# Kernel tuning notes

Measured on AMD Instinct MI355X. Metric: run time of the kernel, lower is better.

The kernel has to match this reference:

```python
import jax, jax.numpy as jnp
import numpy as np

CONF_THRES = 0.8
NMS_THRES = 0.4
MAX_DET = 300          # fixed capacity for jit-compatible NMS output
N_BOXES = 262144
N_CLASSES = 80


def xywh2xyxy(x):
    xy, wh = x[..., :2], x[..., 2:4]
    return jnp.concatenate([xy - wh * 0.5, xy + wh * 0.5], axis=-1)


def bbox_iou(box, boxes):
    # one box [4] vs many [N,4]; original uses the +1 pixel-area convention
    x1 = jnp.maximum(box[0], boxes[:, 0])
    y1 = jnp.maximum(box[1], boxes[:, 1])
    x2 = jnp.minimum(box[2], boxes[:, 2])
    y2 = jnp.minimum(box[3], boxes[:, 3])
    inter = jnp.clip(x2 - x1 + 1, 0) * jnp.clip(y2 - y1 + 1, 0)
    a1 = (box[2] - box[0] + 1) * (box[3] - box[1] + 1)
    a2 = (boxes[:, 2] - boxes[:, 0] + 1) * (boxes[:, 3] - boxes[:, 1] + 1)
    return inter / (a1 + a2 - inter + 1e-16)


def nms_single(pred):
    # pred: [N, 85] raw YOLO output for one image
    boxes = xywh2xyxy(pred[:, :4])
    obj = pred[:, 4]
    cls_scores = pred[:, 5:]
    class_conf = cls_scores.max(axis=-1)
    class_pred = jnp.argmax(cls_scores, axis=-1).astype(pred.dtype)
    valid = obj >= CONF_THRES
    score = obj * class_conf
    # sort valid boxes by descending score; invalid pushed to the end
    order = jnp.argsort(jnp.where(valid, -score, jnp.inf))
    det = jnp.concatenate(
        [boxes, obj[:, None], class_conf[:, None], class_pred[:, None]], axis=1
    )[order]  # [N, 7] = x1,y1,x2,y2,obj,class_conf,class_pred
    valid = valid[order]

    def step(valid, _):
        idx = jnp.argmax(valid)            # first still-valid (= highest score)
        any_valid = jnp.any(valid)
        cur = det[idx]
        iou = bbox_iou(cur[:4], det[:, :4])
        invalid = (iou > NMS_THRES) & (det[:, 6] == cur[6]) & valid
        # weighted box merge over the suppressed group (as in original NMS)
        w = jnp.where(invalid, det[:, 4], 0.0)
        merged = (w[:, None] * det[:, :4]).sum(0) / (w.sum() + 1e-16)
        out = jnp.where(any_valid,
                        jnp.concatenate([merged, cur[4:]]),
                        jnp.zeros(7, pred.dtype))
        return valid & ~invalid, (out, any_valid)

    _, (kept, kept_valid) = jax.lax.scan(step, valid, None, length=MAX_DET)
    return kept, kept_valid  # [MAX_DET,7], [MAX_DET]


def setup_inputs() -> dict:
    key = jax.random.key(0)
    detections = jax.random.uniform(key, (1, N_BOXES, 5 + N_CLASSES), dtype=jnp.float32)
    return {"detections": detections}


def reference(detections):
    kept, kv = nms_single(detections[0])
    d = kept[:, 5:]                        # [MAX_DET, 2] = (class_conf, class_pred)
    conf_key = jnp.where(kv, d[:, 0], -jnp.inf)  # padded rows sort to the end
    order = jnp.argsort(conf_key)          # ascending (torch argsort)
    d = d[order][::-1]                     # torch.flip -> descending class_conf
    kv = kv[order][::-1]
    probs = jnp.where(kv, d[:, 0], 0.0)    # self.probs
    ids = d[:, 1][None, :]                 # self.ids, shape [1, MAX_DET]
    return ids, probs
```

## Files before the change

### kernel.cpp

```cpp
#include <hip/hip_runtime.h>

#pragma clang fp contract(off)

#define NBOX 262144
#define NCLS 80
#define ROWS 85
#define CAP 1024
#define NSUB 8
#define SUBCAP 128
#define POOL 8192

typedef unsigned long long ull;

__global__ __launch_bounds__(1024) void k_init(int* __restrict__ cnt_pad,
                                               int* __restrict__ pool_count) {
    const int t = threadIdx.x;
    for (int i = t; i < NCLS * NSUB * 16; i += 1024) cnt_pad[i] = 0;
    if (t == 0) *pool_count = 0;
}

__global__ __launch_bounds__(256) void k_stage1(const float* __restrict__ det,
                                                int* __restrict__ cnt_pad,
                                                ull* __restrict__ key2,
                                                float* __restrict__ conf2,
                                                float4* __restrict__ box2) {
    __shared__ int s_wl[256];
    __shared__ float s_obj[256];
    __shared__ int wsum[4];
    __shared__ int s_nv;
    const int t = threadIdx.x, lane = t & 63, wave = t >> 6;
    const int bi = blockIdx.x * 256 + t;
    const int sb = blockIdx.x & (NSUB - 1);

    float obj = det[(size_t)bi * ROWS + 4];
    bool valid = (obj >= 0.8f);
    ull m = __ballot(valid);
    if (lane == 0) wsum[wave] = (int)__popcll(m);
    __syncthreads();
    if (t == 0) {
        int s = 0;
        #pragma unroll
        for (int w = 0; w < 4; w++) { int cc = wsum[w]; wsum[w] = s; s += cc; }
        s_nv = s;
    }
    __syncthreads();
    if (valid) {
        int r = wsum[wave] + (int)__popcll(m & ((1ull << lane) - 1ull));
        s_wl[r] = t;
        s_obj[r] = obj;
    }
    __syncthreads();
    const int nv = s_nv;

    const int grp = t >> 4, c = t & 15;
    for (int r0 = 0; r0 < nv; r0 += 16) {
        int widx = r0 + grp;
        if (widx < nv) {
            int b = s_wl[widx];
            const float* p = det + (size_t)(blockIdx.x * 256 + b) * ROWS;
            float aux = (c < 5) ? p[c] : 0.0f;
            float v0 = p[5 + c];
            float v1 = p[21 + c];
            float v2 = p[37 + c];
            float v3 = p[53 + c];
            float v4 = p[69 + c];
            float mv = v0; int mj = c;
            if (v1 > mv) { mv = v1; mj = 16 + c; }
            if (v2 > mv) { mv = v2; mj = 32 + c; }
            if (v3 > mv) { mv = v3; mj = 48 + c; }
            if (v4 > mv) { mv = v4; mj = 64 + c; }
            #pragma unroll
            for (int off = 8; off; off >>= 1) {
                float ov = __shfl_xor(mv, off);
                int oj = __shfl_xor(mj, off);
                if (ov > mv || (ov == mv && oj < mj)) { mv = ov; mj = oj; }
            }
            int gb = lane & 48;
            float x = __shfl(aux, gb + 0);
            float y = __shfl(aux, gb + 1);
            float w = __shfl(aux, gb + 2);
            float h = __shfl(aux, gb + 3);
            if (c == 0) {
                float ob = s_obj[widx];
                float score = ob * mv;
                float hw = w * 0.5f, hh = h * 0.5f;
                int gi = blockIdx.x * 256 + b;
                int r = atomicAdd(&cnt_pad[((mj * NSUB + sb) << 4)], 1);
                if (r < SUBCAP) {
                    int pos = (mj << 10) + (sb << 7) + r;
                    key2[pos] = ((ull)(~__float_as_uint(score)) << 32) | (unsigned)gi;
                    conf2[pos] = mv;
                    box2[pos] = make_float4(x - hw, y - hh, x + hw, y + hh);
                }
            }
        }
    }
}

template <int L>
__device__ __forceinline__ int exact_alive(ull (&k)[L]) {
    int a = 0;
    #pragma unroll
    for (int j = 0; j < L; j++) a += (int)__popcll(__ballot(k[j] != ~0ULL));
    return a;
}

template <int L>
__device__ __forceinline__ void pick_loop(ull (&k)[L], float4 (&bx)[L], float (&cf)[L],
                                          int lane, int& alive, int& np,
                                          ull* pkey, float* pconf, int stopAt) {
    while (alive > stopAt && np < 300) {
        ull lm = k[0]; int lj = 0;
        #pragma unroll
        for (int j = 1; j < L; j++) if (k[j] < lm) { lm = k[j]; lj = j; }
        ull gm = lm;
        #pragma unroll
        for (int off = 32; off; off >>= 1) { ull o = __shfl_xor(gm, off); if (o < gm) gm = o; }
        if (gm == ~0ULL) { alive = 0; break; }
        float4 cb = bx[0]; float cc = cf[0];
        #pragma unroll
        for (int j = 1; j < L; j++) if (j == lj) { cb = bx[j]; cc = cf[j]; }
        ull wb = __ballot(lm == gm);
        int wl2 = (int)__ffsll((long long)wb) - 1;
        cb.x = __shfl(cb.x, wl2); cb.y = __shfl(cb.y, wl2);
        cb.z = __shfl(cb.z, wl2); cb.w = __shfl(cb.w, wl2);
        cc = __shfl(cc, wl2);
        if (lane == 0) { pkey[np] = gm; pconf[np] = cc; }
        np++;
        float a1 = (cb.z - cb.x + 1.0f) * (cb.w - cb.y + 1.0f);
        #pragma unroll
        for (int j = 0; j < L; j++) {
            if (k[j] != ~0ULL) {
                float4 b = bx[j];
                float xx1 = fmaxf(cb.x, b.x), yy1 = fmaxf(cb.y, b.y);
                float xx2 = fminf(cb.z, b.z), yy2 = fminf(cb.w, b.w);
                float iw = xx2 - xx1 + 1.0f, ih = yy2 - yy1 + 1.0f;
                float inter = fmaxf(iw, 0.0f) * fmaxf(ih, 0.0f);
                float a2 = (b.z - b.x + 1.0f) * (b.w - b.y + 1.0f);
                float iou = inter / (a1 + a2 - inter + 1e-16f);
                if (iou > 0.4f) k[j] = ~0ULL;
            }
        }
        if ((np & 7) == 0) alive = exact_alive(k);
    }
}

template <int LF, int LT>
__device__ __forceinline__ void compact_regs(ull (&k)[LF], float4 (&bx)[LF], float (&cf)[LF],
                                             ull (&k2)[LT], float4 (&b2)[LT], float (&c2)[LT],
                                             int lane, int alive,
                                             ull* dk, float4* db, float* dc) {
    int ci = 0;
    #pragma unroll
    for (int j = 0; j < LF; j++) if (k[j] != ~0ULL) ci++;
    int inc = ci;
    for (int off = 1; off < 64; off <<= 1) {
        int o = __shfl_up(inc, off);
        if (lane >= off) inc += o;
    }
    int wp = inc - ci;
    #pragma unroll
    for (int j = 0; j < LF; j++)
        if (k[j] != ~0ULL) { dk[wp] = k[j]; db[wp] = bx[j]; dc[wp] = cf[j]; wp++; }
    #pragma unroll
    for (int j = 0; j < LT; j++) {
        int pos = lane + (j << 6);
        bool ok = pos < alive;
        k2[j] = ok ? dk[pos] : ~0ULL;
        b2[j] = ok ? db[pos] : make_float4(0.f, 0.f, 0.f, 0.f);
        c2[j] = ok ? dc[pos] : 0.0f;
    }
}

__global__ __launch_bounds__(64) void k_nms(const int* __restrict__ cnt_pad,
                                            const ull* __restrict__ key2,
                                            const float* __restrict__ conf2,
                                            const float4* __restrict__ box2,
                                            ull* __restrict__ pool_key,
                                            float* __restrict__ pool_conf,
                                            int* __restrict__ pool_cls,
                                            int* __restrict__ pool_count) {
    __shared__ ull sk[CAP];
    __shared__ float4 sb[CAP];
    __shared__ float sc[CAP];
    __shared__ ull pkey[CAP];
    __shared__ float pconf[CAP];
    const int c = blockIdx.x, lane = threadIdx.x;
    const int s0 = c << 10;

    int cv0 = 0;
    if (lane < NSUB) cv0 = min(cnt_pad[((c * NSUB + lane) << 4)], SUBCAP);
    int ntot = cv0;
    #pragma unroll
    for (int off = 32; off; off >>= 1) ntot += __shfl_xor(ntot, off);

    ull k16[16]; float4 b16[16]; float c16[16];
    #pragma unroll
    for (int j = 0; j < 16; j++) {
        int pos = lane + (j << 6);
        int sub = pos >> 7;
        int lim = __shfl(cv0, sub);
        bool ok = (pos & (SUBCAP - 1)) < lim;
        k16[j] = ok ? key2[s0 + pos] : ~0ULL;
        b16[j] = ok ? box2[s0 + pos] : make_float4(0.f, 0.f, 0.f, 0.f);
        c16[j] = ok ? conf2[s0 + pos] : 0.0f;
    }
    int alive = ntot, np = 0;
    pick_loop<16>(k16, b16, c16, lane, alive, np, pkey, pconf, 256);
    alive = exact_alive(k16);
    ull k4[4]; float4 b4[4]; float c4[4];
    compact_regs<16, 4>(k16, b16, c16, k4, b4, c4, lane, alive, sk, sb, sc);
    pick_loop<4>(k4, b4, c4, lane, alive, np, pkey, pconf, 64);
    alive = exact_alive(k4);
    ull k1[1]; float4 b1[1]; float c1[1];
    compact_regs<4, 1>(k4, b4, c4, k1, b1, c1, lane, alive, sk, sb, sc);
    pick_loop<1>(k1, b1, c1, lane, alive, np, pkey, pconf, 0);

    int npw = min(np, 300);
    int base = 0;
    if (lane == 0 && npw) base = atomicAdd(pool_count, npw);
    base = __shfl(base, 0);
    for (int j = lane; j < npw; j += 64) {
        int pp = base + j;
        if (pp < POOL) {
            ull gm = pkey[j];
            pool_key[pp] = ((ull)((unsigned)(gm >> 32) & 0x7FFFFFFFu) << 32)
                         | ((gm & 0xFFFFFFFFull) << 14) | (ull)pp;
            pool_conf[pp] = pconf[j];
            pool_cls[pp] = c;
        }
    }
}

__device__ __forceinline__ void bsort512(ull (&x)[8], int lane) {
    #pragma unroll
    for (int k = 2; k <= 512; k <<= 1) {
        #pragma unroll
        for (int j = k >> 1; j >= 64; j >>= 1) {
            const int jr = j >> 6;
            #pragma unroll
            for (int r2 = 0; r2 < 8; r2++) {
                if ((r2 & jr) == 0) {
                    const bool asc = (((r2 << 6) & k) == 0);
                    ull a = x[r2], b = x[r2 | jr];
                    if ((a > b) == asc) { x[r2] = b; x[r2 | jr] = a; }
                }
            }
        }
        #pragma unroll
        for (int j = ((k >> 1) > 32 ? 32 : (k >> 1)); j >= 1; j >>= 1) {
            #pragma unroll
            for (int r2 = 0; r2 < 8; r2++) {
                int i = (r2 << 6) + lane;
                bool asc = ((i & k) == 0);
                ull o = __shfl_xor(x[r2], j);
                bool lower = ((lane & j) == 0);
                ull mn = x[r2] < o ? x[r2] : o;
                ull mx2 = x[r2] < o ? o : x[r2];
                x[r2] = (asc == lower) ? mn : mx2;
            }
        }
    }
}

__global__ __launch_bounds__(256) void k_final(const ull* __restrict__ pool_key,
                                               const float* __restrict__ pool_conf,
                                               const int* __restrict__ pool_cls,
                                               const int* __restrict__ pool_count,
                                               float* __restrict__ out) {
    __shared__ int s_red[4];
    __shared__ int s_stat[2];
    __shared__ ull s_mm[8];
    __shared__ ull s_buf[512];
    __shared__ unsigned s_cb[512];
    __shared__ unsigned s_cl[512];
    const int t = threadIdx.x, wave = t >> 6, lane = t & 63;
    const int K = min(*pool_count, POOL);
    ull key[32];
    #pragma unroll
    for (int j = 0; j < 32; j++) {
        int pos = t + (j << 8);
        key[j] = (pos < K) ? pool_key[pos] : ~0ULL;
    }

    const bool selAll = (K <= 511);
    int bsh = 63; ull p = 0;
    if (!selAll) {
        ull mn = ~0ULL, mx = 0;
        #pragma unroll
        for (int j = 0; j < 32; j++) {
            ull kk = key[j];
            if (kk != ~0ULL) { if (kk < mn) mn = kk; if (kk > mx) mx = kk; }
        }
        #pragma unroll
        for (int off = 32; off; off >>= 1) {
            ull on = __shfl_xor(mn, off), ox = __shfl_xor(mx, off);
            if (on < mn) mn = on;
            if (ox > mx) mx = ox;
        }
        if (lane == 0) { s_mm[wave * 2] = mn; s_mm[wave * 2 + 1] = mx; }
        __syncthreads();
        mn = min(min(s_mm[0], s_mm[2]), min(s_mm[4], s_mm[6]));
        mx = max(max(s_mm[1], s_mm[3]), max(s_mm[5], s_mm[7]));
        ull diff = mn ^ mx;
        int hb = 63 - __builtin_clzll(diff);
        int r = 300, cand = K, b = hb;
        p = mn >> (hb + 1);
        while (b >= 13 && cand > 212) {
            int c0 = 0;
            #pragma unroll
            for (int j = 0; j < 32; j++) {
                ull kk = key[j];
                if ((kk >> (b + 1)) == p && (((kk >> b) & 1ull) == 0)) c0++;
            }
            #pragma unroll
            for (int off = 32; off; off >>= 1) c0 += __shfl_xor(c0, off);
            if (lane == 0) s_red[wave] = c0;
            __syncthreads();
            if (t == 0) s_stat[0] = s_red[0] + s_red[1] + s_red[2] + s_red[3];
            __syncthreads();
            int cnt0 = s_stat[0];
            if (r <= cnt0) { cand = cnt0; p = p << 1; }
            else { r -= cnt0; cand -= cnt0; p = (p << 1) | 1ull; }
            b--;
        }
        bsh = b + 1;
    }

    if (t == 0) s_stat[1] = 0;
    __syncthreads();
    int ci = 0;
    #pragma unroll
    for (int j = 0; j < 32; j++) {
        ull kk = key[j];
        bool sel = selAll ? ((kk >> 63) == 0) : ((kk >> bsh) <= p);
        if (sel) ci++;
    }
    int inc = ci;
    for (int off = 1; off < 64; off <<= 1) {
        int o = __shfl_up(inc, off);
        if (lane >= off) inc += o;
    }
    int wtot = __shfl(inc, 63);
    int wbase2 = 0;
    if (lane == 0 && wtot) wbase2 = atomicAdd(&s_stat[1], wtot);
    wbase2 = __shfl(wbase2, 0);
    int wp = wbase2 + inc - ci;
    #pragma unroll
    for (int j = 0; j < 32; j++) {
        ull kk = key[j];
        bool sel = selAll ? ((kk >> 63) == 0) : ((kk >> bsh) <= p);
        if (sel) s_buf[wp++] = kk;
    }
    __syncthreads();
    const int S = s_stat[1];
    for (int i = t; i < 512; i += 256) if (i >= S) s_buf[i] = ~0ULL;
    __syncthreads();
    if (wave != 0) return;

    #pragma clang loop unroll(disable)
    for (int pass = 0; pass < 2; pass++) {
        ull x[8];
        #pragma unroll
        for (int r2 = 0; r2 < 8; r2++) x[r2] = s_buf[(r2 << 6) + lane];
        bsort512(x, lane);
        if (pass == 0) {
            #pragma unroll
            for (int r2 = 0; r2 < 8; r2++) {
                int i = (r2 << 6) + lane;
                ull kk = x[r2];
                ull k2 = ~0ULL;
                if (i < 300 && kk != ~0ULL) {
                    int pidx = (int)(kk & 0x3FFFull);
                    unsigned cb = __float_as_uint(pool_conf[pidx]);
                    unsigned cl = (unsigned)pool_cls[pidx];
                    s_cb[i] = cb; s_cl[i] = cl;
                    k2 = ((ull)(~cb) << 32) | (unsigned)(~i);
                }
                s_buf[i] = k2;
            }
        } else {
            #pragma unroll
            for (int r2 = 0; r2 < 8; r2++) {
                int i = (r2 << 6) + lane;
                if (i < 300) {
                    ull kk = x[r2];
                    float idv = 0.0f, pv = 0.0f;
                    if (kk != ~0ULL) {
                        int slot = (int)(~(unsigned)(kk & 0xFFFFFFFFull));
                        pv = __uint_as_float(s_cb[slot]);
                        idv = (float)(int)s_cl[slot];
                    }
                    out[i] = idv;
                    out[300 + i] = pv;
                }
            }
        }
    }
}

extern "C" void kernel_launch(void* const* d_in, const int* in_sizes, int n_in,
                              void* d_out, int out_size, void* d_ws, size_t ws_size,
                              hipStream_t stream) {
    const float* det = (const float*)d_in[0];
    float* out = (float*)d_out;
    char* ws = (char*)d_ws;

    int* cnt_pad = (int*)(ws + 0);
    int* pool_count = (int*)(ws + 40960);
    ull* key2 = (ull*)(ws + 41024);
    float* conf2 = (float*)(ws + 696384);
    float4* box2 = (float4*)(ws + 1024064);
    ull* pool_key = (ull*)(ws + 2334784);
    float* pool_conf = (float*)(ws + 2400320);
    int* pool_cls = (int*)(ws + 2433088);

    k_init<<<1, 1024, 0, stream>>>(cnt_pad, pool_count);
    k_stage1<<<NBOX / 256, 256, 0, stream>>>(det, cnt_pad, key2, conf2, box2);
    k_nms<<<NCLS, 64, 0, stream>>>(cnt_pad, key2, conf2, box2,
                                   pool_key, pool_conf, pool_cls, pool_count);
    k_final<<<1, 256, 0, stream>>>(pool_key, pool_conf, pool_cls, pool_count, out);
}
```

Baseline: 178.9 us.

## Fuse per-class NMS with final sort via last-block ticket, widen stage1 blocks

Merges the per-class NMS kernel and the final selection kernel into one launch. Every block takes a ticket from a done counter, and the last block to finish runs the final top-k sort. This removes one kernel launch and the gap between launches. Stage1 now has each block handle 1024 boxes with 4 per thread and compacts them through a shared atomic instead of a ballot prefix sum, and box areas are precomputed once per candidate rather than at every IoU step. The costs are that the fused kernel runs 256-thread blocks with only one wave active in the NMS phase, and that the shared-atomic compaction no longer preserves candidate order within a block.

```diff
diff --git a/kernel.cpp b/kernel.cpp
--- a/kernel.cpp
+++ b/kernel.cpp
@@ -9,14 +9,16 @@
 #define NSUB 8
 #define SUBCAP 128
 #define POOL 8192
+#define BPT 4
 
 typedef unsigned long long ull;
 
 __global__ __launch_bounds__(1024) void k_init(int* __restrict__ cnt_pad,
-                                               int* __restrict__ pool_count) {
+                                               int* __restrict__ pool_count,
+                                               int* __restrict__ done_count) {
     const int t = threadIdx.x;
     for (int i = t; i < NCLS * NSUB * 16; i += 1024) cnt_pad[i] = 0;
-    if (t == 0) *pool_count = 0;
+    if (t == 0) { *pool_count = 0; *done_count = 0; }
 }
 
 __global__ __launch_bounds__(256) void k_stage1(const float* __restrict__ det,
@@ -24,40 +26,39 @@
                                                 ull* __restrict__ key2,
                                                 float* __restrict__ conf2,
                                                 float4* __restrict__ box2) {
-    __shared__ int s_wl[256];
-    __shared__ float s_obj[256];
-    __shared__ int wsum[4];
+    __shared__ int s_wl[1024];
+    __shared__ float s_obj[1024];
     __shared__ int s_nv;
-    const int t = threadIdx.x, lane = t & 63, wave = t >> 6;
-    const int bi = blockIdx.x * 256 + t;
+    const int t = threadIdx.x;
+    const int b0 = blockIdx.x * 1024;
     const int sb = blockIdx.x & (NSUB - 1);
 
-    float obj = det[(size_t)bi * ROWS + 4];
-    bool valid = (obj >= 0.8f);
-    ull m = __ballot(valid);
-    if (lane == 0) wsum[wave] = (int)__popcll(m);
-    __syncthreads();
-    if (t == 0) {
-        int s = 0;
-        #pragma unroll
-        for (int w = 0; w < 4; w++) { int cc = wsum[w]; wsum[w] = s; s += cc; }
-        s_nv = s;
-    }
-    __syncthreads();
-    if (valid) {
-        int r = wsum[wave] + (int)__popcll(m & ((1ull << lane) - 1ull));
-        s_wl[r] = t;
-        s_obj[r] = obj;
+    if (t == 0) s_nv = 0;
+    __syncthreads();
+
+    float obj[BPT];
+    #pragma unroll
+    for (int i = 0; i < BPT; i++)
+        obj[i] = det[(size_t)(b0 + (i << 8) + t) * ROWS + 4];
+    #pragma unroll
+    for (int i = 0; i < BPT; i++) {
+        if (obj[i] >= 0.8f) {
+            int r = atomicAdd(&s_nv, 1);
+            s_wl[r] = (i << 8) + t;
+            s_obj[r] = obj[i];
+        }
     }
     __syncthreads();
     const int nv = s_nv;
 
     const int grp = t >> 4, c = t & 15;
+    const int lane = t & 63;
+    #pragma unroll 2
     for (int r0 = 0; r0 < nv; r0 += 16) {
         int widx = r0 + grp;
         if (widx < nv) {
             int b = s_wl[widx];
-            const float* p = det + (size_t)(blockIdx.x * 256 + b) * ROWS;
+            const float* p = det + (size_t)(b0 + b) * ROWS;
             float aux = (c < 5) ? p[c] : 0.0f;
             float v0 = p[5 + c];
             float v1 = p[21 + c];
@@ -84,7 +85,7 @@
                 float ob = s_obj[widx];
                 float score = ob * mv;
                 float hw = w * 0.5f, hh = h * 0.5f;
-                int gi = blockIdx.x * 256 + b;
+                int gi = b0 + b;
                 int r = atomicAdd(&cnt_pad[((mj * NSUB + sb) << 4)], 1);
                 if (r < SUBCAP) {
                     int pos = (mj << 10) + (sb << 7) + r;
@@ -107,6 +108,7 @@
 
 template <int L>
 __device__ __forceinline__ void pick_loop(ull (&k)[L], float4 (&bx)[L], float (&cf)[L],
+                                          float (&ar)[L],
                                           int lane, int& alive, int& np,
                                           ull* pkey, float* pconf, int stopAt) {
     while (alive > stopAt && np < 300) {
@@ -136,8 +138,7 @@
                 float xx2 = fminf(cb.z, b.z), yy2 = fminf(cb.w, b.w);
                 float iw = xx2 - xx1 + 1.0f, ih = yy2 - yy1 + 1.0f;
                 float inter = fmaxf(iw, 0.0f) * fmaxf(ih, 0.0f);
-                float a2 = (b.z - b.x + 1.0f) * (b.w - b.y + 1.0f);
-                float iou = inter / (a1 + a2 - inter + 1e-16f);
+                float iou = inter / (a1 + ar[j] - inter + 1e-16f);
                 if (iou > 0.4f) k[j] = ~0ULL;
             }
         }
@@ -148,6 +149,7 @@
 template <int LF, int LT>
 __device__ __forceinline__ void compact_regs(ull (&k)[LF], float4 (&bx)[LF], float (&cf)[LF],
                                              ull (&k2)[LT], float4 (&b2)[LT], float (&c2)[LT],
+                                             float (&a2)[LT],
                                              int lane, int alive,
                                              ull* dk, float4* db, float* dc) {
     int ci = 0;
@@ -169,66 +171,7 @@
         k2[j] = ok ? dk[pos] : ~0ULL;
         b2[j] = ok ? db[pos] : make_float4(0.f, 0.f, 0.f, 0.f);
         c2[j] = ok ? dc[pos] : 0.0f;
-    }
-}
-
-__global__ __launch_bounds__(64) void k_nms(const int* __restrict__ cnt_pad,
-                                            const ull* __restrict__ key2,
-                                            const float* __restrict__ conf2,
-                                            const float4* __restrict__ box2,
-                                            ull* __restrict__ pool_key,
-                                            float* __restrict__ pool_conf,
-                                            int* __restrict__ pool_cls,
-                                            int* __restrict__ pool_count) {
-    __shared__ ull sk[CAP];
-    __shared__ float4 sb[CAP];
-    __shared__ float sc[CAP];
-    __shared__ ull pkey[CAP];
-    __shared__ float pconf[CAP];
-    const int c = blockIdx.x, lane = threadIdx.x;
-    const int s0 = c << 10;
-
-    int cv0 = 0;
-    if (lane < NSUB) cv0 = min(cnt_pad[((c * NSUB + lane) << 4)], SUBCAP);
-    int ntot = cv0;
-    #pragma unroll
-    for (int off = 32; off; off >>= 1) ntot += __shfl_xor(ntot, off);
-
-    ull k16[16]; float4 b16[16]; float c16[16];
-    #pragma unroll
-    for (int j = 0; j < 16; j++) {
-        int pos = lane + (j << 6);
-        int sub = pos >> 7;
-        int lim = __shfl(cv0, sub);
-        bool ok = (pos & (SUBCAP - 1)) < lim;
-        k16[j] = ok ? key2[s0 + pos] : ~0ULL;
-        b16[j] = ok ? box2[s0 + pos] : make_float4(0.f, 0.f, 0.f, 0.f);
-        c16[j] = ok ? conf2[s0 + pos] : 0.0f;
-    }
-    int alive = ntot, np = 0;
-    pick_loop<16>(k16, b16, c16, lane, alive, np, pkey, pconf, 256);
-    alive = exact_alive(k16);
-    ull k4[4]; float4 b4[4]; float c4[4];
-    compact_regs<16, 4>(k16, b16, c16, k4, b4, c4, lane, alive, sk, sb, sc);
-    pick_loop<4>(k4, b4, c4, lane, alive, np, pkey, pconf, 64);
-    alive = exact_alive(k4);
-    ull k1[1]; float4 b1[1]; float c1[1];
-    compact_regs<4, 1>(k4, b4, c4, k1, b1, c1, lane, alive, sk, sb, sc);
-    pick_loop<1>(k1, b1, c1, lane, alive, np, pkey, pconf, 0);
-
-    int npw = min(np, 300);
-    int base = 0;
-    if (lane == 0 && npw) base = atomicAdd(pool_count, npw);
-    base = __shfl(base, 0);
-    for (int j = lane; j < npw; j += 64) {
-        int pp = base + j;
-        if (pp < POOL) {
-            ull gm = pkey[j];
-            pool_key[pp] = ((ull)((unsigned)(gm >> 32) & 0x7FFFFFFFu) << 32)
-                         | ((gm & 0xFFFFFFFFull) << 14) | (ull)pp;
-            pool_conf[pp] = pconf[j];
-            pool_cls[pp] = c;
-        }
+        a2[j] = (b2[j].z - b2[j].x + 1.0f) * (b2[j].w - b2[j].y + 1.0f);
     }
 }
 
@@ -263,19 +206,88 @@
     }
 }
 
-__global__ __launch_bounds__(256) void k_final(const ull* __restrict__ pool_key,
-                                               const float* __restrict__ pool_conf,
-                                               const int* __restrict__ pool_cls,
-                                               const int* __restrict__ pool_count,
-                                               float* __restrict__ out) {
+__global__ __launch_bounds__(256) void k_nms(const int* __restrict__ cnt_pad,
+                                             const ull* __restrict__ key2,
+                                             const float* __restrict__ conf2,
+                                             const float4* __restrict__ box2,
+                                             ull* __restrict__ pool_key,
+                                             float* __restrict__ pool_conf,
+                                             int* __restrict__ pool_cls,
+                                             int* __restrict__ pool_count,
+                                             int* __restrict__ done_count,
+                                             float* __restrict__ out) {
+    __shared__ ull sk[CAP];
+    __shared__ float4 sbx[CAP];
+    __shared__ float scf[CAP];
+    __shared__ ull pkey[CAP];
+    __shared__ float pconf[CAP];
+    __shared__ int s_fin;
     __shared__ int s_red[4];
     __shared__ int s_stat[2];
     __shared__ ull s_mm[8];
     __shared__ ull s_buf[512];
     __shared__ unsigned s_cb[512];
     __shared__ unsigned s_cl[512];
-    const int t = threadIdx.x, wave = t >> 6, lane = t & 63;
-    const int K = min(*pool_count, POOL);
+
+    const int c = blockIdx.x, t = threadIdx.x, lane = t & 63, wave = t >> 6;
+
+    if (wave == 0) {
+        const int s0 = c << 10;
+        int cv0 = 0;
+        if (lane < NSUB) cv0 = min(cnt_pad[((c * NSUB + lane) << 4)], SUBCAP);
+        int ntot = cv0;
+        #pragma unroll
+        for (int off = 32; off; off >>= 1) ntot += __shfl_xor(ntot, off);
+
+        ull k16[16]; float4 b16[16]; float c16[16]; float a16[16];
+        #pragma unroll
+        for (int j = 0; j < 16; j++) {
+            int pos = lane + (j << 6);
+            int sub = pos >> 7;
+            int lim = __shfl(cv0, sub);
+            bool ok = (pos & (SUBCAP - 1)) < lim;
+            k16[j] = ok ? key2[s0 + pos] : ~0ULL;
+            b16[j] = ok ? box2[s0 + pos] : make_float4(0.f, 0.f, 0.f, 0.f);
+            c16[j] = ok ? conf2[s0 + pos] : 0.0f;
+            a16[j] = (b16[j].z - b16[j].x + 1.0f) * (b16[j].w - b16[j].y + 1.0f);
+        }
+        int alive = ntot, np = 0;
+        pick_loop<16>(k16, b16, c16, a16, lane, alive, np, pkey, pconf, 256);
+        alive = exact_alive(k16);
+        ull k4[4]; float4 b4[4]; float c4[4]; float a4[4];
+        compact_regs<16, 4>(k16, b16, c16, k4, b4, c4, a4, lane, alive, sk, sbx, scf);
+        pick_loop<4>(k4, b4, c4, a4, lane, alive, np, pkey, pconf, 64);
+        alive = exact_alive(k4);
+        ull k1[1]; float4 b1[1]; float c1[1]; float a1r[1];
+        compact_regs<4, 1>(k4, b4, c4, k1, b1, c1, a1r, lane, alive, sk, sbx, scf);
+        pick_loop<1>(k1, b1, c1, a1r, lane, alive, np, pkey, pconf, 0);
+
+        int npw = min(np, 300);
+        int base = 0;
+        if (lane == 0 && npw) base = atomicAdd(pool_count, npw);
+        base = __shfl(base, 0);
+        for (int j = lane; j < npw; j += 64) {
+            int pp = base + j;
+            if (pp < POOL) {
+                ull gm = pkey[j];
+                pool_key[pp] = ((ull)((unsigned)(gm >> 32) & 0x7FFFFFFFu) << 32)
+                             | ((gm & 0xFFFFFFFFull) << 14) | (ull)pp;
+                pool_conf[pp] = pconf[j];
+                pool_cls[pp] = c;
+            }
+        }
+        __threadfence();
+    }
+    __syncthreads();
+    if (t == 0) {
+        int ticket = atomicAdd(done_count, 1);
+        s_fin = (ticket == NCLS - 1) ? 1 : 0;
+    }
+    __syncthreads();
+    if (!s_fin) return;
+    __threadfence();
+
+    const int K = min(atomicAdd(pool_count, 0), POOL);
     ull key[32];
     #pragma unroll
     for (int j = 0; j < 32; j++) {
@@ -408,6 +420,7 @@
 
     int* cnt_pad = (int*)(ws + 0);
     int* pool_count = (int*)(ws + 40960);
+    int* done_count = (int*)(ws + 40964);
     ull* key2 = (ull*)(ws + 41024);
     float* conf2 = (float*)(ws + 696384);
     float4* box2 = (float4*)(ws + 1024064);
@@ -415,9 +428,9 @@
     float* pool_conf = (float*)(ws + 2400320);
     int* pool_cls = (int*)(ws + 2433088);
 
-    k_init<<<1, 1024, 0, stream>>>(cnt_pad, pool_count);
-    k_stage1<<<NBOX / 256, 256, 0, stream>>>(det, cnt_pad, key2, conf2, box2);
-    k_nms<<<NCLS, 64, 0, stream>>>(cnt_pad, key2, conf2, box2,
-                                   pool_key, pool_conf, pool_cls, pool_count);
-    k_final<<<1, 256, 0, stream>>>(pool_key, pool_conf, pool_cls, pool_count, out);
-}
+    k_init<<<1, 1024, 0, stream>>>(cnt_pad, pool_count, done_count);
+    k_stage1<<<NBOX / 1024, 256, 0, stream>>>(det, cnt_pad, key2, conf2, box2);
+    k_nms<<<NCLS, 256, 0, stream>>>(cnt_pad, key2, conf2, box2,
+                                    pool_key, pool_conf, pool_cls, pool_count,
+                                    done_count, out);
+}
```

After: 192.2 us. +7.4%, slower.
